# Kernel optimization log

Hardware: AMD Instinct MI355X
Metric: run time of the kernel (lower is better)

Reference implementation:

```python
import jax, jax.numpy as jnp
import numpy as np

B, C = 2000000, 24

def setup_inputs() -> dict:
    key = jax.random.key(0)
    k1, k2 = jax.random.split(key)
    input = jax.random.normal(k1, (B, C), dtype=jnp.float32)
    target = jax.random.randint(k2, (B, C), 0, 2, dtype=jnp.int32)
    return {"input": input, "target": target}

def reference(input, target):
    # LSEP: loss = log1p( sum_i sum_{p in pos_i, n in neg_i} exp(x_in - x_ip) ) / B
    # The ragged double loop factorizes per row:
    #   sum_{p,n} exp(x_n - x_p) = (sum_n exp(x_n)) * (sum_p exp(-x_p))
    pos = target > 0
    neg = target == 0
    s_neg = jnp.sum(jnp.where(neg, jnp.exp(input), 0.0), axis=1)   # [B]
    s_pos = jnp.sum(jnp.where(pos, jnp.exp(-input), 0.0), axis=1)  # [B]
    total = jnp.sum(s_neg * s_pos)
    batch_size = input.shape[0]
    return jnp.log1p(total) / batch_size
```

## Files before the change

### kernel.cpp

```cpp
#include <hip/hip_runtime.h>
#include <math.h>


constexpr int  ROWS   = 2000000;
constexpr int  BLOCK  = 256;
constexpr int  GRID   = 2048;
constexpr int  K      = 3;
constexpr int  TILE4  = BLOCK * K;
constexpr int  TROWS  = TILE4 / 6;
constexpr int  NTILES = 15625;

__global__ __launch_bounds__(BLOCK) void lsep_main(
        const float4* __restrict__ input,
        const int4*   __restrict__ target,
        double*       __restrict__ partials)
{
    __shared__ float2 pair[2][TILE4];
    __shared__ double sred[BLOCK / 64];

    const int t = threadIdx.x;
    double acc = 0.0;

    int buf = 0;
    for (int tile = blockIdx.x; tile < NTILES; tile += GRID, buf ^= 1) {
        const long base = (long)tile * TILE4;

        const float4 x0 = input[base + t];
        const float4 x1 = input[base + t + BLOCK];
        const float4 x2 = input[base + t + 2 * BLOCK];
        const int4   g0 = target[base + t];
        const int4   g1 = target[base + t + BLOCK];
        const int4   g2 = target[base + t + 2 * BLOCK];

        float2 p0, p1, p2;
        #define LSEP_P4(dst, xv, tv) { \
            float a_ = 0.0f, b_ = 0.0f; \
            { const float e = __expf(__int_as_float(__float_as_int(xv.x) ^ (tv.x << 31))); \
              const float f = (float)tv.x; b_ = fmaf(e, f, b_); a_ = fmaf(e, 1.0f - f, a_); } \
            { const float e = __expf(__int_as_float(__float_as_int(xv.y) ^ (tv.y << 31))); \
              const float f = (float)tv.y; b_ = fmaf(e, f, b_); a_ = fmaf(e, 1.0f - f, a_); } \
            { const float e = __expf(__int_as_float(__float_as_int(xv.z) ^ (tv.z << 31))); \
              const float f = (float)tv.z; b_ = fmaf(e, f, b_); a_ = fmaf(e, 1.0f - f, a_); } \
            { const float e = __expf(__int_as_float(__float_as_int(xv.w) ^ (tv.w << 31))); \
              const float f = (float)tv.w; b_ = fmaf(e, f, b_); a_ = fmaf(e, 1.0f - f, a_); } \
            dst = make_float2(a_, b_); }
        LSEP_P4(p0, x0, g0)
        LSEP_P4(p1, x1, g1)
        LSEP_P4(p2, x2, g2)
        #undef LSEP_P4

        pair[buf][t]             = p0;
        pair[buf][t + BLOCK]     = p1;
        pair[buf][t + 2 * BLOCK] = p2;
        __syncthreads();

        if (t < TROWS) {
            const float4* pr = reinterpret_cast<const float4*>(pair[buf]) + 3 * t;
            const float4 q0 = pr[0], q1 = pr[1], q2 = pr[2];
            const float a = (q0.x + q0.z) + (q1.x + q1.z) + (q2.x + q2.z);
            const float b = (q0.y + q0.w) + (q1.y + q1.w) + (q2.y + q2.w);
            acc += (double)a * (double)b;
        }
    }

    #pragma unroll
    for (int off = 32; off > 0; off >>= 1)
        acc += __shfl_down(acc, off, 64);
    if ((t & 63) == 0) sred[t >> 6] = acc;
    __syncthreads();
    if (t == 0)
        partials[blockIdx.x] = (sred[0] + sred[1]) + (sred[2] + sred[3]);
}

__global__ void lsep_finalize(const double* __restrict__ partials,
                              float* __restrict__ out)
{
    __shared__ double sred[4];
    const int t = threadIdx.x;
    double s = 0.0;
    for (int i = t; i < GRID; i += 256) s += partials[i];
    #pragma unroll
    for (int off = 32; off > 0; off >>= 1)
        s += __shfl_down(s, off, 64);
    if ((t & 63) == 0) sred[t >> 6] = s;
    __syncthreads();
    if (t == 0)
        out[0] = (float)(log1p((sred[0] + sred[1]) + (sred[2] + sred[3])) / (double)ROWS);
}

extern "C" void kernel_launch(void* const* d_in, const int* in_sizes, int n_in,
                              void* d_out, int out_size, void* d_ws, size_t ws_size,
                              hipStream_t stream) {
    const float4* input  = (const float4*)d_in[0];
    const int4*   target = (const int4*)d_in[1];
    double* partials = (double*)d_ws;
    float*  out      = (float*)d_out;

    lsep_main<<<GRID, BLOCK, 0, stream>>>(input, target, partials);
    lsep_finalize<<<1, 256, 0, stream>>>(partials, out);
}
```

Measured before the change: 375.7 us.

## Software-pipeline loads with inline asm and exact 5-tile-per-block grid

Sets the grid to 3125 blocks so each block handles exactly five tiles, and fully unrolls the tile loop. It uses inline-asm global loads with manual vmcnt waits so the next tile's loads are in flight while the current tile is computed. The aim is to hide memory latency and keep more bytes outstanding per wave in this bandwidth-bound reduction. In exchange, the kernel depends on hand-written asm, fixed sizes and careful wait counts, and it uses more registers per thread.

```diff
diff --git a/kernel.cpp b/kernel.cpp
--- a/kernel.cpp
+++ b/kernel.cpp
@@ -4,64 +4,82 @@
 
 constexpr int  ROWS   = 2000000;
 constexpr int  BLOCK  = 256;
-constexpr int  GRID   = 2048;
-constexpr int  K      = 3;
-constexpr int  TILE4  = BLOCK * K;
-constexpr int  TROWS  = TILE4 / 6;
-constexpr int  NTILES = 15625;
+constexpr int  GRID   = 3125;
+constexpr int  TILE4  = 768;
+constexpr long STEP4  = (long)GRID * TILE4;
+
+typedef float f32x4 __attribute__((ext_vector_type(4)));
+typedef int   i32x4 __attribute__((ext_vector_type(4)));
+
+__device__ __forceinline__ float2 pp4(f32x4 x, i32x4 g) {
+    float a = 0.0f, b = 0.0f;
+    #pragma unroll
+    for (int j = 0; j < 4; ++j) {
+        const float e = __expf(__int_as_float(__float_as_int(x[j]) ^ (g[j] << 31)));
+        const float f = (float)g[j];
+        b = fmaf(e, f, b);
+        a = fmaf(e, 1.0f - f, a);
+    }
+    return make_float2(a, b);
+}
+
+#define ISSUE(X, G, B4) do {                                                              \
+    const f32x4* pf_ = fin + (B4) + t;                                                    \
+    const i32x4* pg_ = gin + (B4) + t;                                                    \
+    asm volatile("global_load_dwordx4 %0, %1, off" : "=v"(X[0]) : "v"(pf_)       : "memory"); \
+    asm volatile("global_load_dwordx4 %0, %1, off" : "=v"(X[1]) : "v"(pf_ + 256) : "memory"); \
+    asm volatile("global_load_dwordx4 %0, %1, off" : "=v"(X[2]) : "v"(pf_ + 512) : "memory"); \
+    asm volatile("global_load_dwordx4 %0, %1, off" : "=v"(G[0]) : "v"(pg_)       : "memory"); \
+    asm volatile("global_load_dwordx4 %0, %1, off" : "=v"(G[1]) : "v"(pg_ + 256) : "memory"); \
+    asm volatile("global_load_dwordx4 %0, %1, off" : "=v"(G[2]) : "v"(pg_ + 512) : "memory"); \
+} while (0)
+
+#define WAITV(N) do {                                                 \
+    asm volatile("s_waitcnt vmcnt(" #N ")" ::: "memory");             \
+    __builtin_amdgcn_sched_barrier(0);                                \
+} while (0)
+
+#define LDS_BARRIER() asm volatile("s_waitcnt lgkmcnt(0)\n\ts_barrier" ::: "memory")
+
+#define COMPUTE(X, G, BUF) do {                                                      \
+    const float2 p0_ = pp4(X[0], G[0]);                                              \
+    const float2 p1_ = pp4(X[1], G[1]);                                              \
+    const float2 p2_ = pp4(X[2], G[2]);                                              \
+    pair[BUF][t]       = p0_;                                                        \
+    pair[BUF][t + 256] = p1_;                                                        \
+    pair[BUF][t + 512] = p2_;                                                        \
+    LDS_BARRIER();                                                                   \
+    if (t < 128) {                                                                   \
+        const float4* pr_ = reinterpret_cast<const float4*>(&pair[BUF][0]) + 3 * t;  \
+        const float4 q0_ = pr_[0], q1_ = pr_[1], q2_ = pr_[2];                       \
+        const float a_ = (q0_.x + q0_.z) + (q1_.x + q1_.z) + (q2_.x + q2_.z);        \
+        const float b_ = (q0_.y + q0_.w) + (q1_.y + q1_.w) + (q2_.y + q2_.w);        \
+        acc += (double)a_ * (double)b_;                                              \
+    }                                                                                \
+} while (0)
 
 __global__ __launch_bounds__(BLOCK) void lsep_main(
-        const float4* __restrict__ input,
-        const int4*   __restrict__ target,
-        double*       __restrict__ partials)
+        const f32x4* __restrict__ fin,
+        const i32x4* __restrict__ gin,
+        double*      __restrict__ partials)
 {
-    __shared__ float2 pair[2][TILE4];
+    __shared__ __align__(16) float2 pair[2][TILE4];
     __shared__ double sred[BLOCK / 64];
 
-    const int t = threadIdx.x;
+    const int  t  = threadIdx.x;
+    const long b0 = (long)blockIdx.x * TILE4;
     double acc = 0.0;
 
-    int buf = 0;
-    for (int tile = blockIdx.x; tile < NTILES; tile += GRID, buf ^= 1) {
-        const long base = (long)tile * TILE4;
+    f32x4 XA[3], XB[3];
+    i32x4 GA[3], GB[3];
 
-        const float4 x0 = input[base + t];
-        const float4 x1 = input[base + t + BLOCK];
-        const float4 x2 = input[base + t + 2 * BLOCK];
-        const int4   g0 = target[base + t];
-        const int4   g1 = target[base + t + BLOCK];
-        const int4   g2 = target[base + t + 2 * BLOCK];
+    ISSUE(XA, GA, b0);
 
-        float2 p0, p1, p2;
-        #define LSEP_P4(dst, xv, tv) { \
-            float a_ = 0.0f, b_ = 0.0f; \
-            { const float e = __expf(__int_as_float(__float_as_int(xv.x) ^ (tv.x << 31))); \
-              const float f = (float)tv.x; b_ = fmaf(e, f, b_); a_ = fmaf(e, 1.0f - f, a_); } \
-            { const float e = __expf(__int_as_float(__float_as_int(xv.y) ^ (tv.y << 31))); \
-              const float f = (float)tv.y; b_ = fmaf(e, f, b_); a_ = fmaf(e, 1.0f - f, a_); } \
-            { const float e = __expf(__int_as_float(__float_as_int(xv.z) ^ (tv.z << 31))); \
-              const float f = (float)tv.z; b_ = fmaf(e, f, b_); a_ = fmaf(e, 1.0f - f, a_); } \
-            { const float e = __expf(__int_as_float(__float_as_int(xv.w) ^ (tv.w << 31))); \
-              const float f = (float)tv.w; b_ = fmaf(e, f, b_); a_ = fmaf(e, 1.0f - f, a_); } \
-            dst = make_float2(a_, b_); }
-        LSEP_P4(p0, x0, g0)
-        LSEP_P4(p1, x1, g1)
-        LSEP_P4(p2, x2, g2)
-        #undef LSEP_P4
-
-        pair[buf][t]             = p0;
-        pair[buf][t + BLOCK]     = p1;
-        pair[buf][t + 2 * BLOCK] = p2;
-        __syncthreads();
-
-        if (t < TROWS) {
-            const float4* pr = reinterpret_cast<const float4*>(pair[buf]) + 3 * t;
-            const float4 q0 = pr[0], q1 = pr[1], q2 = pr[2];
-            const float a = (q0.x + q0.z) + (q1.x + q1.z) + (q2.x + q2.z);
-            const float b = (q0.y + q0.w) + (q1.y + q1.w) + (q2.y + q2.w);
-            acc += (double)a * (double)b;
-        }
-    }
+    ISSUE(XB, GB, b0 + 1 * STEP4);  WAITV(6);  COMPUTE(XA, GA, 0);
+    ISSUE(XA, GA, b0 + 2 * STEP4);  WAITV(6);  COMPUTE(XB, GB, 1);
+    ISSUE(XB, GB, b0 + 3 * STEP4);  WAITV(6);  COMPUTE(XA, GA, 0);
+    ISSUE(XA, GA, b0 + 4 * STEP4);  WAITV(6);  COMPUTE(XB, GB, 1);
+                   WAITV(0);  COMPUTE(XA, GA, 0);
 
     #pragma unroll
     for (int off = 32; off > 0; off >>= 1)
@@ -91,11 +109,11 @@
 extern "C" void kernel_launch(void* const* d_in, const int* in_sizes, int n_in,
                               void* d_out, int out_size, void* d_ws, size_t ws_size,
                               hipStream_t stream) {
-    const float4* input  = (const float4*)d_in[0];
-    const int4*   target = (const int4*)d_in[1];
+    const f32x4* fin = (const f32x4*)d_in[0];
+    const i32x4* gin = (const i32x4*)d_in[1];
     double* partials = (double*)d_ws;
     float*  out      = (float*)d_out;
 
-    lsep_main<<<GRID, BLOCK, 0, stream>>>(input, target, partials);
+    lsep_main<<<GRID, BLOCK, 0, stream>>>(fin, gin, partials);
     lsep_finalize<<<1, 256, 0, stream>>>(partials, out);
 }
```

Result: no change. 377.9 us (+0.6%).
